# Kernel optimization log

Measured on AMD Instinct MI355X. Metric: run time of the kernel, lower is better.

## Reference

```python
import jax, jax.numpy as jnp
import numpy as np

N_NODES = 50000
N_EDGES = 800000
D_IN = 256
D_HID = 256
N_LAYERS = 3
N_GRAPHS = 64
LN_EPS = 1e-5


def setup_inputs() -> dict:
    key = jax.random.key(0)
    ks = jax.random.split(key, 8)
    x = jax.random.normal(ks[0], (N_NODES, D_IN), dtype=jnp.float32)
    edge_index = jax.random.randint(ks[1], (2, N_EDGES), 0, N_NODES, dtype=jnp.int32)
    batch = jnp.sort(jax.random.randint(ks[2], (N_NODES,), 0, N_GRAPHS, dtype=jnp.int32))
    # GCNConv weights (glorot-ish) and biases; all layers are [D, D] since in_dim == hidden_dim
    scale = 1.0 / np.sqrt(D_IN)
    Ws = jax.random.normal(ks[3], (N_LAYERS, D_IN, D_HID), dtype=jnp.float32) * scale
    bs = jnp.zeros((N_LAYERS, D_HID), dtype=jnp.float32)
    gammas = jnp.ones((N_LAYERS, D_HID), dtype=jnp.float32)
    betas = jnp.zeros((N_LAYERS, D_HID), dtype=jnp.float32)
    return {"x": x, "edge_index": edge_index, "batch": batch,
            "Ws": Ws, "bs": bs, "gammas": gammas, "betas": betas}


def _gcn_conv(x, W, b, src, dst):
    # PyG GCNConv: h = xW; add self-loops; symmetric deg^{-1/2} normalization; scatter-add; + bias
    h = x @ W  # [N, D]
    deg = jnp.zeros((N_NODES,), dtype=x.dtype).at[dst].add(1.0) + 1.0  # +1 for self-loop
    dinv = jax.lax.rsqrt(deg)  # deg >= 1, safe
    coef = (dinv[src] * dinv[dst])[:, None]  # [E, 1]
    agg = jax.ops.segment_sum(h[src] * coef, dst, num_segments=N_NODES)
    agg = agg + h * (dinv * dinv)[:, None]  # self-loop contribution
    return agg + b


def _layer_norm(x, gamma, beta):
    mu = jnp.mean(x, axis=-1, keepdims=True)
    var = jnp.mean(jnp.square(x - mu), axis=-1, keepdims=True)
    return (x - mu) * jax.lax.rsqrt(var + LN_EPS) * gamma + beta


def reference(x, edge_index, batch, Ws, bs, gammas, betas):
    src, dst = edge_index[0], edge_index[1]
    h = x
    for l in range(N_LAYERS):
        h = _gcn_conv(h, Ws[l], bs[l], src, dst)
        h = _layer_norm(h, gammas[l], betas[l])
        h = jax.nn.relu(h)  # dropout is identity in eval mode
    # global mean pool over graphs
    sums = jax.ops.segment_sum(h, batch, num_segments=N_GRAPHS)  # [B, D]
    counts = jax.ops.segment_sum(jnp.ones((N_NODES,), dtype=h.dtype), batch, num_segments=N_GRAPHS)
    return sums / jnp.maximum(counts, 1.0)[:, None]
```

## Files before the change

kernel.cpp:

```cpp
#include <hip/hip_runtime.h>
#include <hip/hip_bf16.h>

#define N_NODES   50000
#define N_EDGES   800000
#define D         256
#define N_LAYERS  3
#define N_GRAPHS  64
#define LN_EPS    1e-5f
#define NB_SCAN   ((N_NODES + 255) / 256)
#define XT_THREADS (N_NODES * D / 8)

typedef __attribute__((ext_vector_type(8))) short bf16x8;
typedef __attribute__((ext_vector_type(4))) short s16x4;
typedef __attribute__((ext_vector_type(4))) float f32x4;

__device__ __forceinline__ unsigned short f2bf(float f) {
    unsigned int u = __float_as_uint(f);
    unsigned int r = (u + 0x7FFFu + ((u >> 16) & 1u)) >> 16;
    return (unsigned short)r;
}
__device__ __forceinline__ float bf2f(unsigned short h) {
    return __uint_as_float(((unsigned int)h) << 16);
}

__global__ void k_convert(const float* __restrict__ x, const float* __restrict__ dinv,
                          unsigned short* __restrict__ xb,
                          const float* __restrict__ W, unsigned short* __restrict__ Wbt) {
    int gid = blockIdx.x * blockDim.x + threadIdx.x;
    if (gid < XT_THREADS) {
        int base = gid * 8;
        float sc = dinv[base >> 8];
        const float4* x4 = (const float4*)(x + base);
        float4 a = x4[0], b = x4[1];
        ushort4 lo, hi;
        lo.x = f2bf(a.x * sc); lo.y = f2bf(a.y * sc); lo.z = f2bf(a.z * sc); lo.w = f2bf(a.w * sc);
        hi.x = f2bf(b.x * sc); hi.y = f2bf(b.y * sc); hi.z = f2bf(b.z * sc); hi.w = f2bf(b.w * sc);
        ((ushort4*)(xb + base))[0] = lo;
        ((ushort4*)(xb + base))[1] = hi;
    } else {
        int g2 = gid - XT_THREADS;
        if (g2 < N_LAYERS * D * D) {
            int l = g2 >> 16;
            int rem = g2 & 65535;
            int n = rem >> 8;
            int k = rem & 255;
            Wbt[(size_t)l * D * D + n * D + k] = f2bf(W[(size_t)l * D * D + k * D + n]);
        }
    }
}

__global__ void k_indeg(const int* __restrict__ dst, int* __restrict__ indeg) {
    int e = blockIdx.x * blockDim.x + threadIdx.x;
    if (e < N_EDGES) atomicAdd(&indeg[dst[e]], 1);
}

__global__ __launch_bounds__(256) void k_dinv_bsum(const int* __restrict__ indeg,
                                                   float* __restrict__ dinv,
                                                   int* __restrict__ bsum) {
    int b = blockIdx.x, t = threadIdx.x;
    int i = b * 256 + t;
    int v = (i < N_NODES) ? indeg[i] : 0;
    if (i < N_NODES) dinv[i] = rsqrtf((float)(v + 1));
    int s = v;
#pragma unroll
    for (int m = 32; m >= 1; m >>= 1) s += __shfl_xor(s, m);
    __shared__ int sh[4];
    if ((t & 63) == 0) sh[t >> 6] = s;
    __syncthreads();
    if (t == 0) bsum[b] = sh[0] + sh[1] + sh[2] + sh[3];
}

__global__ __launch_bounds__(256) void k_bscan_counts(const int* __restrict__ bsum,
                                                      int* __restrict__ bbase,
                                                      const int* __restrict__ batch,
                                                      int* __restrict__ counts) {
    int t = threadIdx.x;
    if (t < N_GRAPHS) {
        int g = t;
        int lo = 0, hi = N_NODES;
        while (lo < hi) { int mid = (lo + hi) >> 1; if (batch[mid] < g) lo = mid + 1; else hi = mid; }
        int start = lo;
        lo = 0; hi = N_NODES;
        int g1 = g + 1;
        while (lo < hi) { int mid = (lo + hi) >> 1; if (batch[mid] < g1) lo = mid + 1; else hi = mid; }
        counts[g] = lo - start;
    }
    __shared__ int s[256];
    int v = (t < NB_SCAN) ? bsum[t] : 0;
    s[t] = v;
    __syncthreads();
    for (int off = 1; off < 256; off <<= 1) {
        int tv = (t >= off) ? s[t - off] : 0;
        __syncthreads();
        s[t] += tv;
        __syncthreads();
    }
    if (t < NB_SCAN) bbase[t] = s[t] - v;
}

__global__ __launch_bounds__(256) void k_offsets(const int* __restrict__ indeg, const int* __restrict__ bbase,
                                                 int* __restrict__ offsets, int* __restrict__ cursor) {
    __shared__ int s[256];
    int b = blockIdx.x, t = threadIdx.x;
    int i = b * 256 + t;
    int v = (i < N_NODES) ? indeg[i] : 0;
    s[t] = v;
    __syncthreads();
    for (int off = 1; off < 256; off <<= 1) {
        int tv = (t >= off) ? s[t - off] : 0;
        __syncthreads();
        s[t] += tv;
        __syncthreads();
    }
    if (i < N_NODES) {
        int o = bbase[b] + s[t] - v;
        offsets[i] = o;
        cursor[i]  = o;
    }
}

__global__ void k_csr_fill(const int* __restrict__ src, const int* __restrict__ dst,
                           int* __restrict__ cursor, unsigned short* __restrict__ esrc) {
    int e = blockIdx.x * blockDim.x + threadIdx.x;
    if (e >= N_EDGES) return;
    int s = src[e], d = dst[e];
    int pos = atomicAdd(&cursor[d], 1);
    esrc[pos] = (unsigned short)s;
}

__global__ __launch_bounds__(256) void k_agg(const unsigned short* __restrict__ h,
                                             const int* __restrict__ offsets,
                                             const int* __restrict__ indeg,
                                             const float* __restrict__ dinv,
                                             const unsigned short* __restrict__ esrc,
                                             unsigned short* __restrict__ outA) {
    const int node = blockIdx.x * 4 + (threadIdx.x >> 6);
    const int lane = threadIdx.x & 63;
    if (node >= N_NODES) return;
    const int hw = lane >> 5;
    const int dl = lane & 31;
    const unsigned short* hp = h + dl * 8;

    float acc[8];
    if (hw == 0) {
        bf16x8 v = *(const bf16x8*)(hp + (size_t)node * 256);
#pragma unroll
        for (int j = 0; j < 8; ++j) acc[j] = bf2f((unsigned short)v[j]);
    } else {
#pragma unroll
        for (int j = 0; j < 8; ++j) acc[j] = 0.f;
    }

    const int beg = offsets[node];
    const int end = beg + indeg[node];
    int i = beg + hw;
    for (; i + 6 < end; i += 8) {
        int s0 = (int)__builtin_nontemporal_load(esrc + i);
        int s1 = (int)__builtin_nontemporal_load(esrc + i + 2);
        int s2 = (int)__builtin_nontemporal_load(esrc + i + 4);
        int s3 = (int)__builtin_nontemporal_load(esrc + i + 6);
        bf16x8 v0 = *(const bf16x8*)(hp + (size_t)s0 * 256);
        bf16x8 v1 = *(const bf16x8*)(hp + (size_t)s1 * 256);
        bf16x8 v2 = *(const bf16x8*)(hp + (size_t)s2 * 256);
        bf16x8 v3 = *(const bf16x8*)(hp + (size_t)s3 * 256);
#pragma unroll
        for (int j = 0; j < 8; ++j) acc[j] += bf2f((unsigned short)v0[j]);
#pragma unroll
        for (int j = 0; j < 8; ++j) acc[j] += bf2f((unsigned short)v1[j]);
#pragma unroll
        for (int j = 0; j < 8; ++j) acc[j] += bf2f((unsigned short)v2[j]);
#pragma unroll
        for (int j = 0; j < 8; ++j) acc[j] += bf2f((unsigned short)v3[j]);
    }
    for (; i < end; i += 2) {
        int s0 = (int)__builtin_nontemporal_load(esrc + i);
        bf16x8 v0 = *(const bf16x8*)(hp + (size_t)s0 * 256);
#pragma unroll
        for (int j = 0; j < 8; ++j) acc[j] += bf2f((unsigned short)v0[j]);
    }

#pragma unroll
    for (int j = 0; j < 8; ++j) acc[j] += __shfl_xor(acc[j], 32);

    if (hw == 0) {
        float sc = dinv[node];
        bf16x8 o;
#pragma unroll
        for (int j = 0; j < 8; ++j) o[j] = (short)f2bf(acc[j] * sc);
        __builtin_nontemporal_store(o, (bf16x8*)(outA + (size_t)node * 256 + dl * 8));
    }
}

__global__ __launch_bounds__(256, 4) void k_gemm_ln(const unsigned short* __restrict__ A,
                                                    const unsigned short* __restrict__ Wbt,
                                                    const float* __restrict__ bias,
                                                    const float* __restrict__ gamma,
                                                    const float* __restrict__ beta,
                                                    const float* __restrict__ rowscale,
                                                    unsigned short* __restrict__ out) {
    __shared__ float red[2][4][32];
    const int t = threadIdx.x;
    const int lane = t & 63;
    const int w = t >> 6;
    const int lrow = lane & 15;
    const int q = lane >> 4;
    const int mbase = blockIdx.x * 32;
    const int ncb = w * 64;

    int rowA[2];
#pragma unroll
    for (int mt = 0; mt < 2; ++mt) {
        int r = mbase + mt * 16 + lrow;
        rowA[mt] = (r < N_NODES) ? r : (N_NODES - 1);
    }
    const unsigned short* a0 = A + (size_t)rowA[0] * 256 + q * 8;
    const unsigned short* a1 = A + (size_t)rowA[1] * 256 + q * 8;
    const unsigned short* wp = Wbt + (size_t)(ncb + lrow) * 256 + q * 8;

    f32x4 acc[2][4];
#pragma unroll
    for (int mt = 0; mt < 2; ++mt)
#pragma unroll
        for (int nt = 0; nt < 4; ++nt) acc[mt][nt] = (f32x4){0.f, 0.f, 0.f, 0.f};

#pragma unroll
    for (int ks = 0; ks < 8; ++ks) {
        bf16x8 av0 = *(const bf16x8*)(a0 + ks * 32);
        bf16x8 av1 = *(const bf16x8*)(a1 + ks * 32);
#pragma unroll
        for (int nt = 0; nt < 4; ++nt) {
            bf16x8 b = *(const bf16x8*)(wp + (size_t)nt * 16 * 256 + ks * 32);
            acc[0][nt] = __builtin_amdgcn_mfma_f32_16x16x32_bf16(b, av0, acc[0][nt], 0, 0, 0);
            acc[1][nt] = __builtin_amdgcn_mfma_f32_16x16x32_bf16(b, av1, acc[1][nt], 0, 0, 0);
        }
    }

    const float4* bias4 = (const float4*)bias;
#pragma unroll
    for (int mt = 0; mt < 2; ++mt) {
        float s = 0.f, s2 = 0.f;
#pragma unroll
        for (int nt = 0; nt < 4; ++nt) {
            float4 bv = bias4[w * 16 + nt * 4 + q];
#pragma unroll
            for (int r = 0; r < 4; ++r) {
                float v = acc[mt][nt][r] + ((const float*)&bv)[r];
                acc[mt][nt][r] = v;
                s += v;
                s2 += v * v;
            }
        }
        s  += __shfl_xor(s, 16);  s  += __shfl_xor(s, 32);
        s2 += __shfl_xor(s2, 16); s2 += __shfl_xor(s2, 32);
        if (lane < 16) {
            red[0][w][mt * 16 + lane] = s;
            red[1][w][mt * 16 + lane] = s2;
        }
    }
    __syncthreads();

    const float4* g4 = (const float4*)gamma;
    const float4* be4 = (const float4*)beta;
#pragma unroll
    for (int mt = 0; mt < 2; ++mt) {
        int r = mt * 16 + lrow;
        float s = 0.f, s2 = 0.f;
#pragma unroll
        for (int j = 0; j < 4; ++j) { s += red[0][j][r]; s2 += red[1][j][r]; }
        float mu = s * (1.0f / 256.0f);
        float var = s2 * (1.0f / 256.0f) - mu * mu;
        float rs = rsqrtf(var + LN_EPS);

        int row = mbase + r;
        if (row < N_NODES) {
            float sc = (rowscale != nullptr) ? rowscale[row] : 1.0f;
#pragma unroll
            for (int nt = 0; nt < 4; ++nt) {
                float4 gv = g4[w * 16 + nt * 4 + q];
                float4 bev = be4[w * 16 + nt * 4 + q];
                s16x4 o;
                float v0 = fmaxf((acc[mt][nt][0] - mu) * rs * gv.x + bev.x, 0.f) * sc;
                float v1 = fmaxf((acc[mt][nt][1] - mu) * rs * gv.y + bev.y, 0.f) * sc;
                float v2 = fmaxf((acc[mt][nt][2] - mu) * rs * gv.z + bev.z, 0.f) * sc;
                float v3 = fmaxf((acc[mt][nt][3] - mu) * rs * gv.w + bev.w, 0.f) * sc;
                o[0] = (short)f2bf(v0); o[1] = (short)f2bf(v1);
                o[2] = (short)f2bf(v2); o[3] = (short)f2bf(v3);
                __builtin_nontemporal_store(o, (s16x4*)(out + (size_t)row * 256 + ncb + nt * 16 + q * 4));
            }
        }
    }
}

__global__ __launch_bounds__(256) void k_pool(const unsigned short* __restrict__ h,
                                              const int* __restrict__ batch,
                                              float* __restrict__ sums) {
    __shared__ int sb[128];
    int t = threadIdx.x;
    int n0 = blockIdx.x * 128;
    int cnt = N_NODES - n0; if (cnt > 128) cnt = 128;
    if (cnt <= 0) return;
    if (t < cnt) sb[t] = batch[n0 + t];
    __syncthreads();

    int half = t >> 7;
    int c2 = t & 127;
    float ax = 0.f, ay = 0.f;
    int g = (half < cnt) ? sb[half] : -1;
    for (int i = half; i < cnt; i += 2) {
        int bg = sb[i];
        if (bg != g) {
            atomicAdd(&sums[g * 256 + c2 * 2], ax);
            atomicAdd(&sums[g * 256 + c2 * 2 + 1], ay);
            ax = ay = 0.f;
            g = bg;
        }
        ushort2 v = *(const ushort2*)(h + (size_t)(n0 + i) * 256 + c2 * 2);
        ax += bf2f(v.x);
        ay += bf2f(v.y);
    }
    if (g >= 0) {
        atomicAdd(&sums[g * 256 + c2 * 2], ax);
        atomicAdd(&sums[g * 256 + c2 * 2 + 1], ay);
    }
}

__global__ void k_finalize(const float* __restrict__ sums, const int* __restrict__ counts,
                           float* __restrict__ out) {
    int idx = blockIdx.x * blockDim.x + threadIdx.x;
    if (idx < N_GRAPHS * 256) {
        float c = (float)counts[idx >> 8];
        out[idx] = sums[idx] / fmaxf(c, 1.f);
    }
}

extern "C" void kernel_launch(void* const* d_in, const int* in_sizes, int n_in,
                              void* d_out, int out_size, void* d_ws, size_t ws_size,
                              hipStream_t stream) {
    const float* x     = (const float*)d_in[0];
    const int*   ei    = (const int*)d_in[1];
    const int*   batch = (const int*)d_in[2];
    const float* Ws    = (const float*)d_in[3];
    const float* bs    = (const float*)d_in[4];
    const float* gammas= (const float*)d_in[5];
    const float* betas = (const float*)d_in[6];
    float* out = (float*)d_out;

    const int* src = ei;
    const int* dst = ei + N_EDGES;

    char* p = (char*)d_ws;
    unsigned short* hbf   = (unsigned short*)p; p += (size_t)N_NODES * D * 2;
    unsigned short* aggx  = (unsigned short*)p; p += (size_t)N_NODES * D * 2;
    unsigned short* Wbt   = (unsigned short*)p; p += (size_t)N_LAYERS * D * D * 2;
    int*   indeg  = (int*)p;   p += (size_t)N_NODES * 4;
    int*   offs   = (int*)p;   p += (size_t)N_NODES * 4;
    int*   cursor = (int*)p;   p += (size_t)N_NODES * 4;
    float* dinv   = (float*)p; p += (size_t)N_NODES * 4;
    int*   bsum   = (int*)p;   p += (size_t)NB_SCAN * 4;
    int*   bbase  = (int*)p;   p += (size_t)NB_SCAN * 4;
    unsigned short* esrc = (unsigned short*)p; p += (size_t)N_EDGES * 2;
    float* sums   = (float*)p; p += (size_t)N_GRAPHS * D * 4;
    int*   counts = (int*)p;   p += (size_t)N_GRAPHS * 4;

    hipMemsetAsync(indeg, 0, (size_t)N_NODES * 4, stream);
    hipMemsetAsync(sums, 0, (size_t)N_GRAPHS * D * 4, stream);

    k_indeg <<<(N_EDGES + 255) / 256, 256, 0, stream>>>(dst, indeg);
    k_dinv_bsum<<<NB_SCAN, 256, 0, stream>>>(indeg, dinv, bsum);
    k_convert<<<(XT_THREADS + N_LAYERS * D * D + 255) / 256, 256, 0, stream>>>(x, dinv, hbf, Ws, Wbt);
    k_bscan_counts<<<1, 256, 0, stream>>>(bsum, bbase, batch, counts);
    k_offsets<<<NB_SCAN, 256, 0, stream>>>(indeg, bbase, offs, cursor);
    k_csr_fill<<<(N_EDGES + 255) / 256, 256, 0, stream>>>(src, dst, cursor, esrc);

    const int agg_grid  = (N_NODES + 3) / 4;
    const int gemm_grid = (N_NODES + 31) / 32;
    for (int l = 0; l < N_LAYERS; ++l) {
        k_agg<<<agg_grid, 256, 0, stream>>>(hbf, offs, indeg, dinv, esrc, aggx);
        const float* rsc = (l == N_LAYERS - 1) ? nullptr : dinv;
        k_gemm_ln<<<gemm_grid, 256, 0, stream>>>(aggx, Wbt + (size_t)l * D * D,
                                                 bs + (size_t)l * D,
                                                 gammas + (size_t)l * D,
                                                 betas + (size_t)l * D, rsc, hbf);
    }

    k_pool<<<(N_NODES + 127) / 128, 256, 0, stream>>>(hbf, batch, sums);
    k_finalize<<<(N_GRAPHS * 256 + 255) / 256, 256, 0, stream>>>(sums, counts, out);
}
```

Baseline: 485.0 us.

## Fuse neighbor aggregation with GEMM+LayerNorm in one per-layer kernel via LDS

Merges the gather/aggregate kernel and the GEMM+LayerNorm kernel into a single per-layer kernel. Each 32-row block first aggregates its nodes into a swizzled LDS tile, then runs MFMA against W fragments preloaded into registers. This removes the intermediate aggregated-activation round trip through global memory and one launch per layer, and adds ping-pong activation buffers so no layer reads the buffer it writes. The pool kernel is also simplified to one column per thread, and nontemporal loads/stores are dropped. The cost is larger LDS use and register pressure, which can lower occupancy for the latency-bound gather phase.

```diff
diff --git a/kernel.cpp b/kernel.cpp
--- a/kernel.cpp
+++ b/kernel.cpp
@@ -11,7 +11,6 @@
 #define XT_THREADS (N_NODES * D / 8)
 
 typedef __attribute__((ext_vector_type(8))) short bf16x8;
-typedef __attribute__((ext_vector_type(4))) short s16x4;
 typedef __attribute__((ext_vector_type(4))) float f32x4;
 
 __device__ __forceinline__ unsigned short f2bf(float f) {
@@ -128,110 +127,116 @@
     esrc[pos] = (unsigned short)s;
 }
 
-__global__ __launch_bounds__(256) void k_agg(const unsigned short* __restrict__ h,
-                                             const int* __restrict__ offsets,
-                                             const int* __restrict__ indeg,
-                                             const float* __restrict__ dinv,
-                                             const unsigned short* __restrict__ esrc,
-                                             unsigned short* __restrict__ outA) {
-    const int node = blockIdx.x * 4 + (threadIdx.x >> 6);
-    const int lane = threadIdx.x & 63;
-    if (node >= N_NODES) return;
-    const int hw = lane >> 5;
-    const int dl = lane & 31;
-    const unsigned short* hp = h + dl * 8;
-
-    float acc[8];
-    if (hw == 0) {
-        bf16x8 v = *(const bf16x8*)(hp + (size_t)node * 256);
-#pragma unroll
-        for (int j = 0; j < 8; ++j) acc[j] = bf2f((unsigned short)v[j]);
-    } else {
-#pragma unroll
-        for (int j = 0; j < 8; ++j) acc[j] = 0.f;
-    }
-
-    const int beg = offsets[node];
-    const int end = beg + indeg[node];
-    int i = beg + hw;
-    for (; i + 6 < end; i += 8) {
-        int s0 = (int)__builtin_nontemporal_load(esrc + i);
-        int s1 = (int)__builtin_nontemporal_load(esrc + i + 2);
-        int s2 = (int)__builtin_nontemporal_load(esrc + i + 4);
-        int s3 = (int)__builtin_nontemporal_load(esrc + i + 6);
-        bf16x8 v0 = *(const bf16x8*)(hp + (size_t)s0 * 256);
-        bf16x8 v1 = *(const bf16x8*)(hp + (size_t)s1 * 256);
-        bf16x8 v2 = *(const bf16x8*)(hp + (size_t)s2 * 256);
-        bf16x8 v3 = *(const bf16x8*)(hp + (size_t)s3 * 256);
-#pragma unroll
-        for (int j = 0; j < 8; ++j) acc[j] += bf2f((unsigned short)v0[j]);
-#pragma unroll
-        for (int j = 0; j < 8; ++j) acc[j] += bf2f((unsigned short)v1[j]);
-#pragma unroll
-        for (int j = 0; j < 8; ++j) acc[j] += bf2f((unsigned short)v2[j]);
-#pragma unroll
-        for (int j = 0; j < 8; ++j) acc[j] += bf2f((unsigned short)v3[j]);
-    }
-    for (; i < end; i += 2) {
-        int s0 = (int)__builtin_nontemporal_load(esrc + i);
-        bf16x8 v0 = *(const bf16x8*)(hp + (size_t)s0 * 256);
-#pragma unroll
-        for (int j = 0; j < 8; ++j) acc[j] += bf2f((unsigned short)v0[j]);
-    }
-
-#pragma unroll
-    for (int j = 0; j < 8; ++j) acc[j] += __shfl_xor(acc[j], 32);
-
-    if (hw == 0) {
-        float sc = dinv[node];
-        bf16x8 o;
-#pragma unroll
-        for (int j = 0; j < 8; ++j) o[j] = (short)f2bf(acc[j] * sc);
-        __builtin_nontemporal_store(o, (bf16x8*)(outA + (size_t)node * 256 + dl * 8));
-    }
-}
-
-__global__ __launch_bounds__(256, 4) void k_gemm_ln(const unsigned short* __restrict__ A,
-                                                    const unsigned short* __restrict__ Wbt,
-                                                    const float* __restrict__ bias,
-                                                    const float* __restrict__ gamma,
-                                                    const float* __restrict__ beta,
-                                                    const float* __restrict__ rowscale,
-                                                    unsigned short* __restrict__ out) {
+__global__ __launch_bounds__(256) void k_layer(const unsigned short* __restrict__ hs,
+                                               const int* __restrict__ offsets,
+                                               const int* __restrict__ indeg,
+                                               const float* __restrict__ dinv,
+                                               const unsigned short* __restrict__ esrc,
+                                               const unsigned short* __restrict__ Wbt,
+                                               const float* __restrict__ bias,
+                                               const float* __restrict__ gamma,
+                                               const float* __restrict__ beta,
+                                               const float* __restrict__ rowscale,
+                                               unsigned short* __restrict__ out) {
+    __shared__ short alds[32 * 256];
     __shared__ float red[2][4][32];
     const int t = threadIdx.x;
     const int lane = t & 63;
     const int w = t >> 6;
+    const int brow = blockIdx.x * 32;
+
+    const int hw = lane >> 5;
+    const int dl = lane & 31;
+    const unsigned short* hp = hs + dl * 8;
+
+    for (int nn = 0; nn < 8; ++nn) {
+        int node = brow + w * 8 + nn;
+        int nodec = (node < N_NODES) ? node : (N_NODES - 1);
+
+        float acc[8];
+        if (hw == 0) {
+            bf16x8 v = *(const bf16x8*)(hp + (size_t)nodec * 256);
+#pragma unroll
+            for (int j = 0; j < 8; ++j) acc[j] = bf2f((unsigned short)v[j]);
+        } else {
+#pragma unroll
+            for (int j = 0; j < 8; ++j) acc[j] = 0.f;
+        }
+
+        const int beg = offsets[nodec];
+        const int end = beg + indeg[nodec];
+        int i = beg + hw;
+        for (; i + 6 < end; i += 8) {
+            int s0 = esrc[i];
+            int s1 = esrc[i + 2];
+            int s2 = esrc[i + 4];
+            int s3 = esrc[i + 6];
+            bf16x8 v0 = *(const bf16x8*)(hp + (size_t)s0 * 256);
+            bf16x8 v1 = *(const bf16x8*)(hp + (size_t)s1 * 256);
+            bf16x8 v2 = *(const bf16x8*)(hp + (size_t)s2 * 256);
+            bf16x8 v3 = *(const bf16x8*)(hp + (size_t)s3 * 256);
+#pragma unroll
+            for (int j = 0; j < 8; ++j) acc[j] += bf2f((unsigned short)v0[j]);
+#pragma unroll
+            for (int j = 0; j < 8; ++j) acc[j] += bf2f((unsigned short)v1[j]);
+#pragma unroll
+            for (int j = 0; j < 8; ++j) acc[j] += bf2f((unsigned short)v2[j]);
+#pragma unroll
+            for (int j = 0; j < 8; ++j) acc[j] += bf2f((unsigned short)v3[j]);
+        }
+        for (; i < end; i += 2) {
+            int s0 = esrc[i];
+            bf16x8 v0 = *(const bf16x8*)(hp + (size_t)s0 * 256);
+#pragma unroll
+            for (int j = 0; j < 8; ++j) acc[j] += bf2f((unsigned short)v0[j]);
+        }
+
+#pragma unroll
+        for (int j = 0; j < 8; ++j) acc[j] += __shfl_xor(acc[j], 32);
+
+        if (hw == 0) {
+            int r = w * 8 + nn;
+            float sc = dinv[nodec];
+            bf16x8 o;
+#pragma unroll
+            for (int j = 0; j < 8; ++j) o[j] = (short)f2bf(acc[j] * sc);
+            *(bf16x8*)(alds + r * 256 + (dl ^ (r & 7)) * 8) = o;
+        }
+    }
+    __syncthreads();
+
     const int lrow = lane & 15;
     const int q = lane >> 4;
-    const int mbase = blockIdx.x * 32;
     const int ncb = w * 64;
 
-    int rowA[2];
-#pragma unroll
-    for (int mt = 0; mt < 2; ++mt) {
-        int r = mbase + mt * 16 + lrow;
-        rowA[mt] = (r < N_NODES) ? r : (N_NODES - 1);
-    }
-    const unsigned short* a0 = A + (size_t)rowA[0] * 256 + q * 8;
-    const unsigned short* a1 = A + (size_t)rowA[1] * 256 + q * 8;
+    f32x4 acc[2][4];
+#pragma unroll
+    for (int mt = 0; mt < 2; ++mt)
+#pragma unroll
+        for (int nt = 0; nt < 4; ++nt) acc[mt][nt] = (f32x4){0.f, 0.f, 0.f, 0.f};
+
     const unsigned short* wp = Wbt + (size_t)(ncb + lrow) * 256 + q * 8;
 
-    f32x4 acc[2][4];
-#pragma unroll
-    for (int mt = 0; mt < 2; ++mt)
-#pragma unroll
-        for (int nt = 0; nt < 4; ++nt) acc[mt][nt] = (f32x4){0.f, 0.f, 0.f, 0.f};
-
-#pragma unroll
-    for (int ks = 0; ks < 8; ++ks) {
-        bf16x8 av0 = *(const bf16x8*)(a0 + ks * 32);
-        bf16x8 av1 = *(const bf16x8*)(a1 + ks * 32);
-#pragma unroll
-        for (int nt = 0; nt < 4; ++nt) {
-            bf16x8 b = *(const bf16x8*)(wp + (size_t)nt * 16 * 256 + ks * 32);
-            acc[0][nt] = __builtin_amdgcn_mfma_f32_16x16x32_bf16(b, av0, acc[0][nt], 0, 0, 0);
-            acc[1][nt] = __builtin_amdgcn_mfma_f32_16x16x32_bf16(b, av1, acc[1][nt], 0, 0, 0);
+#pragma unroll
+    for (int kh = 0; kh < 2; ++kh) {
+        bf16x8 wf[4][4];
+#pragma unroll
+        for (int nt = 0; nt < 4; ++nt)
+#pragma unroll
+            for (int ks = 0; ks < 4; ++ks)
+                wf[nt][ks] = *(const bf16x8*)(wp + (size_t)nt * 16 * 256 + (kh * 4 + ks) * 32);
+
+#pragma unroll
+        for (int ks = 0; ks < 4; ++ks) {
+            int kk = kh * 4 + ks;
+            int cs = (kk * 4 + q) ^ (lrow & 7);
+#pragma unroll
+            for (int mt = 0; mt < 2; ++mt) {
+                bf16x8 av = *(const bf16x8*)(alds + (mt * 16 + lrow) * 256 + cs * 8);
+#pragma unroll
+                for (int nt = 0; nt < 4; ++nt)
+                    acc[mt][nt] = __builtin_amdgcn_mfma_f32_16x16x32_bf16(wf[nt][ks], av, acc[mt][nt], 0, 0, 0);
+            }
         }
     }
 
@@ -271,21 +276,20 @@
         float var = s2 * (1.0f / 256.0f) - mu * mu;
         float rs = rsqrtf(var + LN_EPS);
 
-        int row = mbase + r;
+        int row = brow + r;
         if (row < N_NODES) {
             float sc = (rowscale != nullptr) ? rowscale[row] : 1.0f;
 #pragma unroll
             for (int nt = 0; nt < 4; ++nt) {
                 float4 gv = g4[w * 16 + nt * 4 + q];
                 float4 bev = be4[w * 16 + nt * 4 + q];
-                s16x4 o;
+                ushort4 o;
                 float v0 = fmaxf((acc[mt][nt][0] - mu) * rs * gv.x + bev.x, 0.f) * sc;
                 float v1 = fmaxf((acc[mt][nt][1] - mu) * rs * gv.y + bev.y, 0.f) * sc;
                 float v2 = fmaxf((acc[mt][nt][2] - mu) * rs * gv.z + bev.z, 0.f) * sc;
                 float v3 = fmaxf((acc[mt][nt][3] - mu) * rs * gv.w + bev.w, 0.f) * sc;
-                o[0] = (short)f2bf(v0); o[1] = (short)f2bf(v1);
-                o[2] = (short)f2bf(v2); o[3] = (short)f2bf(v3);
-                __builtin_nontemporal_store(o, (s16x4*)(out + (size_t)row * 256 + ncb + nt * 16 + q * 4));
+                o.x = f2bf(v0); o.y = f2bf(v1); o.z = f2bf(v2); o.w = f2bf(v3);
+                *(ushort4*)(out + (size_t)row * 256 + ncb + nt * 16 + q * 4) = o;
             }
         }
     }
@@ -302,26 +306,18 @@
     if (t < cnt) sb[t] = batch[n0 + t];
     __syncthreads();
 
-    int half = t >> 7;
-    int c2 = t & 127;
-    float ax = 0.f, ay = 0.f;
-    int g = (half < cnt) ? sb[half] : -1;
-    for (int i = half; i < cnt; i += 2) {
+    float acc = 0.f;
+    int g = sb[0];
+    for (int i = 0; i < cnt; ++i) {
         int bg = sb[i];
         if (bg != g) {
-            atomicAdd(&sums[g * 256 + c2 * 2], ax);
-            atomicAdd(&sums[g * 256 + c2 * 2 + 1], ay);
-            ax = ay = 0.f;
+            atomicAdd(&sums[g * 256 + t], acc);
+            acc = 0.f;
             g = bg;
         }
-        ushort2 v = *(const ushort2*)(h + (size_t)(n0 + i) * 256 + c2 * 2);
-        ax += bf2f(v.x);
-        ay += bf2f(v.y);
-    }
-    if (g >= 0) {
-        atomicAdd(&sums[g * 256 + c2 * 2], ax);
-        atomicAdd(&sums[g * 256 + c2 * 2 + 1], ay);
-    }
+        acc += bf2f(h[(size_t)(n0 + i) * 256 + t]);
+    }
+    atomicAdd(&sums[g * 256 + t], acc);
 }
 
 __global__ void k_finalize(const float* __restrict__ sums, const int* __restrict__ counts,
@@ -349,8 +345,8 @@
     const int* dst = ei + N_EDGES;
 
     char* p = (char*)d_ws;
-    unsigned short* hbf   = (unsigned short*)p; p += (size_t)N_NODES * D * 2;
-    unsigned short* aggx  = (unsigned short*)p; p += (size_t)N_NODES * D * 2;
+    unsigned short* hbfA  = (unsigned short*)p; p += (size_t)N_NODES * D * 2;
+    unsigned short* hbfB  = (unsigned short*)p; p += (size_t)N_NODES * D * 2;
     unsigned short* Wbt   = (unsigned short*)p; p += (size_t)N_LAYERS * D * D * 2;
     int*   indeg  = (int*)p;   p += (size_t)N_NODES * 4;
     int*   offs   = (int*)p;   p += (size_t)N_NODES * 4;
@@ -367,22 +363,25 @@
 
     k_indeg <<<(N_EDGES + 255) / 256, 256, 0, stream>>>(dst, indeg);
     k_dinv_bsum<<<NB_SCAN, 256, 0, stream>>>(indeg, dinv, bsum);
-    k_convert<<<(XT_THREADS + N_LAYERS * D * D + 255) / 256, 256, 0, stream>>>(x, dinv, hbf, Ws, Wbt);
+    k_convert<<<(XT_THREADS + N_LAYERS * D * D + 255) / 256, 256, 0, stream>>>(x, dinv, hbfA, Ws, Wbt);
     k_bscan_counts<<<1, 256, 0, stream>>>(bsum, bbase, batch, counts);
     k_offsets<<<NB_SCAN, 256, 0, stream>>>(indeg, bbase, offs, cursor);
     k_csr_fill<<<(N_EDGES + 255) / 256, 256, 0, stream>>>(src, dst, cursor, esrc);
 
-    const int agg_grid  = (N_NODES + 3) / 4;
-    const int gemm_grid = (N_NODES + 31) / 32;
+    const int layer_grid = (N_NODES + 31) / 32;
+    unsigned short* bufs[2] = {hbfA, hbfB};
     for (int l = 0; l < N_LAYERS; ++l) {
-        k_agg<<<agg_grid, 256, 0, stream>>>(hbf, offs, indeg, dinv, esrc, aggx);
+        const unsigned short* in_h = bufs[l & 1];
+        unsigned short* out_h      = bufs[(l + 1) & 1];
         const float* rsc = (l == N_LAYERS - 1) ? nullptr : dinv;
-        k_gemm_ln<<<gemm_grid, 256, 0, stream>>>(aggx, Wbt + (size_t)l * D * D,
-                                                 bs + (size_t)l * D,
-                                                 gammas + (size_t)l * D,
-                                                 betas + (size_t)l * D, rsc, hbf);
-    }
-
-    k_pool<<<(N_NODES + 127) / 128, 256, 0, stream>>>(hbf, batch, sums);
+        k_layer<<<layer_grid, 256, 0, stream>>>(in_h, offs, indeg, dinv, esrc,
+                                                Wbt + (size_t)l * D * D,
+                                                bs + (size_t)l * D,
+                                                gammas + (size_t)l * D,
+                                                betas + (size_t)l * D, rsc, out_h);
+    }
+
+    unsigned short* hfin = bufs[N_LAYERS & 1];
+    k_pool<<<(N_NODES + 127) / 128, 256, 0, stream>>>(hfin, batch, sums);
     k_finalize<<<(N_GRAPHS * 256 + 255) / 256, 256, 0, stream>>>(sums, counts, out);
 }
```

After: 451.5 us (median of 2 runs). 6.9% less time.
